# Kernel tuning notes

Hardware: AMD Instinct MI355X
Metric: run time of the kernel (lower is better)

## Reference

```python
import jax, jax.numpy as jnp
import numpy as np

TAU = 0.2
NUM_SAMPLES = 8192
EMBED = 64


def setup_inputs() -> dict:
    key = jax.random.key(0)
    k1, k2, k3, k4 = jax.random.split(key, 4)
    all_users = jax.random.normal(k1, (100000, EMBED), dtype=jnp.float32)
    all_items = jax.random.normal(k2, (50000, EMBED), dtype=jnp.float32)
    user_index = jax.random.randint(k3, (NUM_SAMPLES,), 0, 100000, dtype=jnp.int64 if jax.config.jax_enable_x64 else jnp.int32)
    item_index = jax.random.randint(k4, (NUM_SAMPLES,), 0, 50000, dtype=jnp.int64 if jax.config.jax_enable_x64 else jnp.int32)
    return {"all_users": all_users, "all_items": all_items,
            "user_index": user_index, "item_index": item_index}


def _ssm_loss(embed, tau):
    # ratings: [N, N] similarity; positive is the diagonal (self-similarity).
    ratings = jnp.matmul(embed, embed.T) / tau            # [N, N]
    diag = jnp.sum(embed * embed, axis=1) / tau           # diag of embed@embed.T, no NxN gather
    # -log( exp(diag) / sum_j exp(ratings_ij) ) = logsumexp_row - diag
    lse = jax.scipy.special.logsumexp(ratings, axis=1)    # [N]
    return jnp.mean(lse - diag)


def reference(all_users, all_items, user_index, item_index):
    selected_users = all_users[user_index]                # [N, d]
    selected_items = all_items[item_index]                # [N, d]
    loss_u = _ssm_loss(selected_users, TAU)
    loss_i = _ssm_loss(selected_items, TAU)
    inv_loss = loss_u + loss_i
    return inv_loss, jnp.stack([loss_u, loss_i])
```

## Files before the change

kernel.cpp:

```cpp
#include <hip/hip_runtime.h>

#define EMBED    64
#define NS       8192
#define INV_TAU  5.0f
#define NTILE    256
#define JCHUNKS  8
#define JT_PER_CHUNK 32

typedef _Float16 half8  __attribute__((ext_vector_type(8)));
typedef float    f32x16 __attribute__((ext_vector_type(16)));

#define GLDS16(g, l) __builtin_amdgcn_global_load_lds( \
    (const __attribute__((address_space(1))) void*)(g), \
    (__attribute__((address_space(3))) void*)(l), 16, 0, 0)

__global__ __launch_bounds__(256) void prep_kernel(
    const float* __restrict__ users, const float* __restrict__ items,
    const int* __restrict__ uidx, const int* __restrict__ iidx,
    _Float16* __restrict__ Efrag, float* __restrict__ diag) {
  int b = blockIdx.x;
  int mat = b >> 8, tile = b & 255;
  int t = threadIdx.x;
  int row8 = t >> 3, c8 = t & 7;
  int row = tile * 32 + row8;
  int src = mat ? iidx[row] : uidx[row];
  const float4* base = (const float4*)((mat ? items : users) + (size_t)src * EMBED);
  float4 v0 = base[c8 * 2], v1 = base[c8 * 2 + 1];

  __shared__ __align__(16) _Float16 Lh[32][64];
  __shared__ __align__(16) _Float16 Ll[32][64];

  float vs[8] = {v0.x, v0.y, v0.z, v0.w, v1.x, v1.y, v1.z, v1.w};
  float p = 0.f;
  #pragma unroll
  for (int j = 0; j < 8; ++j) {
    float v = vs[j];
    _Float16 h = (_Float16)v;
    _Float16 l = (_Float16)(v - (float)h);
    Lh[row8][c8 * 8 + j] = h;
    Ll[row8][c8 * 8 + j] = l;
    p = fmaf(v, v, p);
  }
  p += __shfl_xor(p, 1);
  p += __shfl_xor(p, 2);
  p += __shfl_xor(p, 4);
  if (c8 == 0) diag[mat * NS + row] = p;
  __syncthreads();

  #pragma unroll
  for (int s = t; s < 512; s += 256) {
    int f = s >> 6, lam = s & 63;
    int hl = f >> 2, kt = f & 3;
    int rr = lam & 31, k0 = kt * 16 + (lam >> 5) * 8;
    const _Float16* Lsrc = hl ? &Ll[0][0] : &Lh[0][0];
    half8 val = *(const half8*)(Lsrc + rr * 64 + k0);
    *(half8*)(Efrag + (((size_t)(mat * NTILE + tile) * 8 + f) * 64 + lam) * 8) = val;
  }
}

__global__ __launch_bounds__(256) void ssm_mfma_kernel(
    const _Float16* __restrict__ Efrag, const float* __restrict__ diag,
    float* __restrict__ rowpart) {
  int b = blockIdx.x;
  int jc  = b & (JCHUNKS - 1);
  int rb  = (b >> 3) & 63;
  int mat = b >> 9;
  int wave = threadIdx.x >> 6;
  int lane = threadIdx.x & 63;
  int hf   = lane >> 5;

  int rowtile = rb * 4 + wave;
  int rowbase = rowtile * 32;

  const _Float16* Em = Efrag + (size_t)mat * NTILE * 8 * 512;

  half8 a[8];
  #pragma unroll
  for (int f = 0; f < 8; ++f)
    a[f] = *(const half8*)(Em + (((size_t)rowtile * 8 + f) * 64 + lane) * 8);

  float dv[16];
  #pragma unroll
  for (int r = 0; r < 16; ++r) {
    int rowl = (r & 3) + 8 * (r >> 2) + 4 * hf;
    dv[r] = diag[mat * NS + rowbase + rowl];
  }

  float rs[16];
  #pragma unroll
  for (int r = 0; r < 16; ++r) rs[r] = 0.f;

  __shared__ __align__(16) _Float16 Bbuf[2][8][64][8];

  int jt0 = jc * JT_PER_CHUNK;
  auto stage = [&](int buf, int jt) {
    const char* src = (const char*)(Em + (size_t)(jt0 + jt) * 8 * 512);
    char* dst = (char*)&Bbuf[buf][0][0][0];
    int o = wave * 2048;
    GLDS16(src + o + lane * 16, dst + o);
    GLDS16(src + o + 1024 + lane * 16, dst + o + 1024);
  };

  stage(0, 0);
  __syncthreads();

  for (int jt = 0; jt < JT_PER_CHUNK; ++jt) {
    int cur = jt & 1;
    if (jt + 1 < JT_PER_CHUNK) stage(cur ^ 1, jt + 1);

    half8 bh[4], bl[4];
    #pragma unroll
    for (int kt = 0; kt < 4; ++kt) {
      bh[kt] = *(const half8*)&Bbuf[cur][kt][lane][0];
      bl[kt] = *(const half8*)&Bbuf[cur][4 + kt][lane][0];
    }

    f32x16 acc = {0.f,0.f,0.f,0.f,0.f,0.f,0.f,0.f,
                  0.f,0.f,0.f,0.f,0.f,0.f,0.f,0.f};
    #pragma unroll
    for (int kt = 0; kt < 4; ++kt)
      acc = __builtin_amdgcn_mfma_f32_32x32x16_f16(a[kt], bh[kt], acc, 0, 0, 0);
    #pragma unroll
    for (int kt = 0; kt < 4; ++kt)
      acc = __builtin_amdgcn_mfma_f32_32x32x16_f16(a[kt], bl[kt], acc, 0, 0, 0);
    #pragma unroll
    for (int kt = 0; kt < 4; ++kt)
      acc = __builtin_amdgcn_mfma_f32_32x32x16_f16(a[4 + kt], bh[kt], acc, 0, 0, 0);

    #pragma unroll
    for (int r = 0; r < 16; ++r)
      rs[r] += __expf((acc[r] - dv[r]) * INV_TAU);

    __syncthreads();
  }

  #pragma unroll
  for (int r = 0; r < 16; ++r) {
    float v = rs[r];
    v += __shfl_xor(v, 16);
    v += __shfl_xor(v, 8);
    v += __shfl_xor(v, 4);
    v += __shfl_xor(v, 2);
    v += __shfl_xor(v, 1);
    if ((lane & 31) == 0) {
      int rowl = (r & 3) + 8 * (r >> 2) + 4 * hf;
      rowpart[jc * (2 * NS) + mat * NS + rowbase + rowl] = v;
    }
  }
}

__global__ __launch_bounds__(1024) void finalize_kernel(
    const float* __restrict__ rowpart, float* __restrict__ out) {
  float lu = 0.f, li = 0.f;
  for (int r = threadIdx.x; r < 2 * NS; r += 1024) {
    float s = 0.f;
    #pragma unroll
    for (int c = 0; c < JCHUNKS; ++c) s += rowpart[c * (2 * NS) + r];
    float l = logf(s);
    if (r < NS) lu += l; else li += l;
  }
  #pragma unroll
  for (int off = 32; off; off >>= 1) {
    lu += __shfl_down(lu, off);
    li += __shfl_down(li, off);
  }
  __shared__ float red[2][16];
  int wave = threadIdx.x >> 6;
  if ((threadIdx.x & 63) == 0) { red[0][wave] = lu; red[1][wave] = li; }
  __syncthreads();
  if (threadIdx.x == 0) {
    float su = 0.f, si = 0.f;
    #pragma unroll
    for (int w = 0; w < 16; ++w) { su += red[0][w]; si += red[1][w]; }
    su *= (1.0f / NS);
    si *= (1.0f / NS);
    out[0] = su + si;
    out[1] = su;
    out[2] = si;
  }
}

extern "C" void kernel_launch(void* const* d_in, const int* in_sizes, int n_in,
                              void* d_out, int out_size, void* d_ws, size_t ws_size,
                              hipStream_t stream) {
  const float* users = (const float*)d_in[0];
  const float* items = (const float*)d_in[1];
  const int*   uidx  = (const int*)d_in[2];
  const int*   iidx  = (const int*)d_in[3];
  float* out = (float*)d_out;

  _Float16* Efrag = (_Float16*)d_ws;
  float* diag     = (float*)((char*)d_ws + (size_t)2 * NTILE * 8 * 512 * 2);
  float* rowpart  = diag + 2 * NS;

  prep_kernel<<<2 * NTILE, 256, 0, stream>>>(users, items, uidx, iidx, Efrag, diag);
  ssm_mfma_kernel<<<2 * 64 * JCHUNKS, 256, 0, stream>>>(Efrag, diag, rowpart);
  finalize_kernel<<<1, 1024, 0, stream>>>(rowpart, out);
}
```

Before: 144.7 us.

## Write MFMA fragments directly in prep, use exp2 with fma, split finalize

```diff
diff --git a/kernel.cpp b/kernel.cpp
--- a/kernel.cpp
+++ b/kernel.cpp
@@ -1,11 +1,11 @@
 #include <hip/hip_runtime.h>
 
-#define EMBED    64
-#define NS       8192
-#define INV_TAU  5.0f
-#define NTILE    256
-#define JCHUNKS  8
+#define EMBED        64
+#define NS           8192
+#define NTILE        256
+#define JCHUNKS      8
 #define JT_PER_CHUNK 32
+#define C_L2E_TAU    7.21347520444482f
 
 typedef _Float16 half8  __attribute__((ext_vector_type(8)));
 typedef float    f32x16 __attribute__((ext_vector_type(16)));
@@ -20,42 +20,39 @@
     _Float16* __restrict__ Efrag, float* __restrict__ diag) {
   int b = blockIdx.x;
   int mat = b >> 8, tile = b & 255;
-  int t = threadIdx.x;
-  int row8 = t >> 3, c8 = t & 7;
-  int row = tile * 32 + row8;
+  int kt = threadIdx.x >> 6;
+  int lane = threadIdx.x & 63;
+  int r = lane & 31;
+  int k0 = kt * 16 + (lane >> 5) * 8;
+  int row = tile * 32 + r;
   int src = mat ? iidx[row] : uidx[row];
-  const float4* base = (const float4*)((mat ? items : users) + (size_t)src * EMBED);
-  float4 v0 = base[c8 * 2], v1 = base[c8 * 2 + 1];
-
-  __shared__ __align__(16) _Float16 Lh[32][64];
-  __shared__ __align__(16) _Float16 Ll[32][64];
-
+  const float4* basep =
+      (const float4*)((mat ? items : users) + (size_t)src * EMBED + k0);
+  float4 v0 = basep[0], v1 = basep[1];
   float vs[8] = {v0.x, v0.y, v0.z, v0.w, v1.x, v1.y, v1.z, v1.w};
+
+  half8 hh, ll;
   float p = 0.f;
   #pragma unroll
   for (int j = 0; j < 8; ++j) {
     float v = vs[j];
     _Float16 h = (_Float16)v;
-    _Float16 l = (_Float16)(v - (float)h);
-    Lh[row8][c8 * 8 + j] = h;
-    Ll[row8][c8 * 8 + j] = l;
+    hh[j] = h;
+    ll[j] = (_Float16)(v - (float)h);
     p = fmaf(v, v, p);
   }
-  p += __shfl_xor(p, 1);
-  p += __shfl_xor(p, 2);
-  p += __shfl_xor(p, 4);
-  if (c8 == 0) diag[mat * NS + row] = p;
+  _Float16* tb = Efrag + (size_t)(mat * NTILE + tile) * 4096;
+  *(half8*)(tb + ((kt)     * 64 + lane) * 8) = hh;
+  *(half8*)(tb + ((4 + kt) * 64 + lane) * 8) = ll;
+
+  p += __shfl_xor(p, 32);
+  __shared__ float ds[4][32];
+  if (lane < 32) ds[kt][lane] = p;
   __syncthreads();
-
-  #pragma unroll
-  for (int s = t; s < 512; s += 256) {
-    int f = s >> 6, lam = s & 63;
-    int hl = f >> 2, kt = f & 3;
-    int rr = lam & 31, k0 = kt * 16 + (lam >> 5) * 8;
-    const _Float16* Lsrc = hl ? &Ll[0][0] : &Lh[0][0];
-    half8 val = *(const half8*)(Lsrc + rr * 64 + k0);
-    *(half8*)(Efrag + (((size_t)(mat * NTILE + tile) * 8 + f) * 64 + lam) * 8) = val;
-  }
+  if (threadIdx.x < 32)
+    diag[mat * NS + tile * 32 + threadIdx.x] =
+        ds[0][threadIdx.x] + ds[1][threadIdx.x] +
+        ds[2][threadIdx.x] + ds[3][threadIdx.x];
 }
 
 __global__ __launch_bounds__(256) void ssm_mfma_kernel(
@@ -71,34 +68,31 @@
 
   int rowtile = rb * 4 + wave;
   int rowbase = rowtile * 32;
-
-  const _Float16* Em = Efrag + (size_t)mat * NTILE * 8 * 512;
+  const _Float16* Em = Efrag + (size_t)mat * NTILE * 4096;
 
   half8 a[8];
   #pragma unroll
   for (int f = 0; f < 8; ++f)
-    a[f] = *(const half8*)(Em + (((size_t)rowtile * 8 + f) * 64 + lane) * 8);
-
-  float dv[16];
-  #pragma unroll
-  for (int r = 0; r < 16; ++r) {
-    int rowl = (r & 3) + 8 * (r >> 2) + 4 * hf;
-    dv[r] = diag[mat * NS + rowbase + rowl];
-  }
+    a[f] = *(const half8*)(Em + (size_t)rowtile * 4096 + (f * 64 + lane) * 8);
+
+  float negdvC[16];
+  #pragma unroll
+  for (int r = 0; r < 16; ++r)
+    negdvC[r] = -diag[mat * NS + rowbase + (r & 3) + 8 * (r >> 2) + 4 * hf]
+                * C_L2E_TAU;
 
   float rs[16];
   #pragma unroll
   for (int r = 0; r < 16; ++r) rs[r] = 0.f;
 
-  __shared__ __align__(16) _Float16 Bbuf[2][8][64][8];
+  __shared__ __align__(16) _Float16 Bbuf[2][4096];
 
   int jt0 = jc * JT_PER_CHUNK;
   auto stage = [&](int buf, int jt) {
-    const char* src = (const char*)(Em + (size_t)(jt0 + jt) * 8 * 512);
-    char* dst = (char*)&Bbuf[buf][0][0][0];
-    int o = wave * 2048;
-    GLDS16(src + o + lane * 16, dst + o);
-    GLDS16(src + o + 1024 + lane * 16, dst + o + 1024);
+    const char* src = (const char*)(Em + (size_t)(jt0 + jt) * 4096) + wave * 2048;
+    char* dst = (char*)&Bbuf[buf][0] + wave * 2048;
+    GLDS16(src + lane * 16, dst);
+    GLDS16(src + 1024 + lane * 16, dst + 1024);
   };
 
   stage(0, 0);
@@ -110,26 +104,28 @@
 
     half8 bh[4], bl[4];
     #pragma unroll
-    for (int kt = 0; kt < 4; ++kt) {
-      bh[kt] = *(const half8*)&Bbuf[cur][kt][lane][0];
-      bl[kt] = *(const half8*)&Bbuf[cur][4 + kt][lane][0];
+    for (int k = 0; k < 4; ++k) {
+      bh[k] = *(const half8*)(&Bbuf[cur][0] + ((k)     * 64 + lane) * 8);
+      bl[k] = *(const half8*)(&Bbuf[cur][0] + ((4 + k) * 64 + lane) * 8);
     }
 
     f32x16 acc = {0.f,0.f,0.f,0.f,0.f,0.f,0.f,0.f,
                   0.f,0.f,0.f,0.f,0.f,0.f,0.f,0.f};
-    #pragma unroll
-    for (int kt = 0; kt < 4; ++kt)
-      acc = __builtin_amdgcn_mfma_f32_32x32x16_f16(a[kt], bh[kt], acc, 0, 0, 0);
-    #pragma unroll
-    for (int kt = 0; kt < 4; ++kt)
-      acc = __builtin_amdgcn_mfma_f32_32x32x16_f16(a[kt], bl[kt], acc, 0, 0, 0);
-    #pragma unroll
-    for (int kt = 0; kt < 4; ++kt)
-      acc = __builtin_amdgcn_mfma_f32_32x32x16_f16(a[4 + kt], bh[kt], acc, 0, 0, 0);
+    __builtin_amdgcn_s_setprio(1);
+    #pragma unroll
+    for (int k = 0; k < 4; ++k)
+      acc = __builtin_amdgcn_mfma_f32_32x32x16_f16(a[k], bh[k], acc, 0, 0, 0);
+    #pragma unroll
+    for (int k = 0; k < 4; ++k)
+      acc = __builtin_amdgcn_mfma_f32_32x32x16_f16(a[k], bl[k], acc, 0, 0, 0);
+    #pragma unroll
+    for (int k = 0; k < 4; ++k)
+      acc = __builtin_amdgcn_mfma_f32_32x32x16_f16(a[4 + k], bh[k], acc, 0, 0, 0);
+    __builtin_amdgcn_s_setprio(0);
 
     #pragma unroll
     for (int r = 0; r < 16; ++r)
-      rs[r] += __expf((acc[r] - dv[r]) * INV_TAU);
+      rs[r] += __builtin_exp2f(fmaf(acc[r], C_L2E_TAU, negdvC[r]));
 
     __syncthreads();
   }
@@ -142,38 +138,41 @@
     v += __shfl_xor(v, 4);
     v += __shfl_xor(v, 2);
     v += __shfl_xor(v, 1);
-    if ((lane & 31) == 0) {
-      int rowl = (r & 3) + 8 * (r >> 2) + 4 * hf;
-      rowpart[jc * (2 * NS) + mat * NS + rowbase + rowl] = v;
-    }
-  }
-}
-
-__global__ __launch_bounds__(1024) void finalize_kernel(
-    const float* __restrict__ rowpart, float* __restrict__ out) {
-  float lu = 0.f, li = 0.f;
-  for (int r = threadIdx.x; r < 2 * NS; r += 1024) {
-    float s = 0.f;
-    #pragma unroll
-    for (int c = 0; c < JCHUNKS; ++c) s += rowpart[c * (2 * NS) + r];
-    float l = logf(s);
-    if (r < NS) lu += l; else li += l;
-  }
+    if ((lane & 31) == 0)
+      rowpart[jc * (2 * NS) + mat * NS + rowbase +
+              (r & 3) + 8 * (r >> 2) + 4 * hf] = v;
+  }
+}
+
+__global__ __launch_bounds__(256) void fin1_kernel(
+    const float* __restrict__ rowpart, float* __restrict__ partial) {
+  int r = blockIdx.x * 256 + threadIdx.x;
+  float s = 0.f;
+  #pragma unroll
+  for (int c = 0; c < JCHUNKS; ++c) s += rowpart[c * (2 * NS) + r];
+  float l = logf(s);
+  #pragma unroll
+  for (int off = 32; off; off >>= 1) l += __shfl_down(l, off);
+  __shared__ float ps[4];
+  if ((threadIdx.x & 63) == 0) ps[threadIdx.x >> 6] = l;
+  __syncthreads();
+  if (threadIdx.x == 0) partial[blockIdx.x] = ps[0] + ps[1] + ps[2] + ps[3];
+}
+
+__global__ __launch_bounds__(64) void fin2_kernel(
+    const float* __restrict__ partial, float* __restrict__ out) {
+  int t = threadIdx.x;
+  float v = partial[t];
+  float vu = (t < 32) ? v : 0.f;
+  float vi = (t < 32) ? 0.f : v;
   #pragma unroll
   for (int off = 32; off; off >>= 1) {
-    lu += __shfl_down(lu, off);
-    li += __shfl_down(li, off);
-  }
-  __shared__ float red[2][16];
-  int wave = threadIdx.x >> 6;
-  if ((threadIdx.x & 63) == 0) { red[0][wave] = lu; red[1][wave] = li; }
-  __syncthreads();
-  if (threadIdx.x == 0) {
-    float su = 0.f, si = 0.f;
-    #pragma unroll
-    for (int w = 0; w < 16; ++w) { su += red[0][w]; si += red[1][w]; }
-    su *= (1.0f / NS);
-    si *= (1.0f / NS);
+    vu += __shfl_down(vu, off);
+    vi += __shfl_down(vi, off);
+  }
+  if (t == 0) {
+    float su = vu * (1.0f / NS);
+    float si = vi * (1.0f / NS);
     out[0] = su + si;
     out[1] = su;
     out[2] = si;
@@ -190,10 +189,12 @@
   float* out = (float*)d_out;
 
   _Float16* Efrag = (_Float16*)d_ws;
-  float* diag     = (float*)((char*)d_ws + (size_t)2 * NTILE * 8 * 512 * 2);
+  float* diag     = (float*)((char*)d_ws + (size_t)4194304);
   float* rowpart  = diag + 2 * NS;
+  float* partial  = (float*)d_ws;
 
   prep_kernel<<<2 * NTILE, 256, 0, stream>>>(users, items, uidx, iidx, Efrag, diag);
   ssm_mfma_kernel<<<2 * 64 * JCHUNKS, 256, 0, stream>>>(Efrag, diag, rowpart);
-  finalize_kernel<<<1, 1024, 0, stream>>>(rowpart, out);
-}
+  fin1_kernel<<<64, 256, 0, stream>>>(rowpart, partial);
+  fin2_kernel<<<1, 64, 0, stream>>>(partial, out);
+}
```

Measured after the change: 151.6 us. +4.8%, slower.
